# Kernel optimization log

Hardware: AMD Instinct MI355X
Metric: run time of the kernel (lower is better)

## Reference

```python
import jax, jax.numpy as jnp
import numpy as np

NUM_HEADS = 8
AREA = 4
EPS = 1e-5  # torch BatchNorm2d default


def _conv1x1(x, w):
    # x: [B,C,H,W], w: [O,C] -> [B,O,H,W]
    return jnp.einsum('bchw,oc->bohw', x, w)


def _bn(y, g, b, m, v):
    # inference-mode BatchNorm2d, per-channel affine
    s = g / jnp.sqrt(v + EPS)
    return y * s[None, :, None, None] + (b - m * s)[None, :, None, None]


def setup_inputs() -> dict:
    key = jax.random.key(0)
    ks = jax.random.split(key, 16)
    B, C, H, W = 2, 256, 64, 64
    d = {}
    d['x'] = jax.random.normal(ks[0], (B, C, H, W), jnp.float32)
    # qk conv (dim -> 2*dim) + BN
    d['w_qk'] = jax.random.normal(ks[1], (2 * C, C), jnp.float32) * 0.06
    d['g_qk'] = jax.random.uniform(ks[2], (2 * C,), jnp.float32, 0.5, 1.5)
    d['b_qk'] = jax.random.normal(ks[3], (2 * C,), jnp.float32) * 0.1
    d['m_qk'] = jax.random.normal(ks[4], (2 * C,), jnp.float32) * 0.1
    d['v_qk'] = jax.random.uniform(ks[5], (2 * C,), jnp.float32, 0.5, 1.5)
    # v conv (dim -> dim) + BN
    d['w_v'] = jax.random.normal(ks[6], (C, C), jnp.float32) * 0.06
    d['g_v'] = jax.random.uniform(ks[7], (C,), jnp.float32, 0.5, 1.5)
    d['b_v'] = jax.random.normal(ks[8], (C,), jnp.float32) * 0.1
    d['m_v'] = jax.random.normal(ks[9], (C,), jnp.float32) * 0.1
    d['v_v'] = jax.random.uniform(ks[10], (C,), jnp.float32, 0.5, 1.5)
    # proj conv (dim -> dim) + BN
    d['w_p'] = jax.random.normal(ks[11], (C, C), jnp.float32) * 0.06
    d['g_p'] = jax.random.uniform(ks[12], (C,), jnp.float32, 0.5, 1.5)
    d['b_p'] = jax.random.normal(ks[13], (C,), jnp.float32) * 0.1
    d['m_p'] = jax.random.normal(ks[14], (C,), jnp.float32) * 0.1
    d['v_p'] = jax.random.uniform(ks[15], (C,), jnp.float32, 0.5, 1.5)
    return d


def reference(x, w_qk, g_qk, b_qk, m_qk, v_qk,
              w_v, g_v, b_v, m_v, v_v,
              w_p, g_p, b_p, m_p, v_p):
    B, C, H, W = x.shape
    N = H * W
    hd = C // NUM_HEADS

    qk = _bn(_conv1x1(x, w_qk), g_qk, b_qk, m_qk, v_qk)          # [B,2C,H,W]
    qk = qk.reshape(B, 2 * C, N).transpose(0, 2, 1)               # [B,N,2C]
    vv = _bn(_conv1x1(x, w_v), g_v, b_v, m_v, v_v)                # [B,C,H,W]
    vv = vv.reshape(B, C, N).transpose(0, 2, 1)                   # [B,N,C]

    Ba, Na = B * AREA, N // AREA
    qk = qk.reshape(Ba, Na, 2 * C)
    vv = vv.reshape(Ba, Na, C)
    q, k = qk[..., :C], qk[..., C:]

    # [Ba,Na,C] -> [Ba,heads,hd,Na] (matches torch transpose(1,2).view)
    q = q.reshape(Ba, Na, NUM_HEADS, hd).transpose(0, 2, 3, 1)
    k = k.reshape(Ba, Na, NUM_HEADS, hd).transpose(0, 2, 3, 1)
    v = vv.reshape(Ba, Na, NUM_HEADS, hd).transpose(0, 2, 3, 1)

    scale = hd ** -0.5
    attn = jnp.einsum('bhdi,bhdj->bhij', q, k) * scale            # [Ba,h,Na,Na]
    attn = jax.nn.softmax(attn, axis=-1)                          # max-sub exp/sum
    out = jnp.einsum('bhdj,bhij->bihd', v, attn)                  # [Ba,Na,h,hd]

    out = out.reshape(B, N, C).reshape(B, H, W, C).transpose(0, 3, 1, 2)
    return _bn(_conv1x1(out, w_p), g_p, b_p, m_p, v_p)            # [B,C,H,W]
```

## Files before the change

### kernel.cpp

```cpp
#include <hip/hip_runtime.h>
#include <hip/hip_bf16.h>
#include <math.h>

#define CCH   256
#define NPIX  4096
#define NHD   8
#define HD    32
#define NA    1024
#define BN_EPS 1e-5f
#define ATT_SCALE (0.17677669529663687f * 1.4426950408889634f)

typedef __attribute__((ext_vector_type(8))) short bf16x8;
typedef __attribute__((ext_vector_type(4))) short bf16x4;
typedef __attribute__((ext_vector_type(4))) float f32x4;

static __device__ inline short f2bf(float f) {
    union { float f; unsigned u; } v; v.f = f;
    unsigned r = (v.u + 0x7fff + ((v.u >> 16) & 1)) >> 16;
    return (short)r;
}

static __device__ inline unsigned int pk2bf(float a, float b) {
    __hip_bfloat162 h2 = __float22bfloat162_rn(make_float2(a, b));
    union { __hip_bfloat162 h; unsigned int u; } v; v.h = h2;
    return v.u;
}

__global__ __launch_bounds__(256)
void prep_kernel(const float* __restrict__ x, short* __restrict__ Xt,
                 const float* __restrict__ wqk, const float* __restrict__ wv,
                 const float* __restrict__ wp, short* __restrict__ Wb) {
    __shared__ short tile[64][66];
    const int t = threadIdx.x;
    const int z = blockIdx.z;
    if (z == 2) {
        const int id  = blockIdx.y * 64 + blockIdx.x;
        const int idx = (id * 256 + t) * 4;
        const float* src; int off;
        if (idx < 131072)      { src = wqk; off = idx; }
        else if (idx < 196608) { src = wv;  off = idx - 131072; }
        else                   { src = wp;  off = idx - 196608; }
        const float4 v = *(const float4*)(src + off);
        short4 o;
        o.x = f2bf(v.x); o.y = f2bf(v.y); o.z = f2bf(v.z); o.w = f2bf(v.w);
        *(short4*)(Wb + idx) = o;
        return;
    }
    const int n0 = blockIdx.x << 6;
    const int c0 = blockIdx.y << 6;
    const int b  = z;
    const float* xp = x + (((size_t)(b * CCH + c0)) << 12) + n0;
    #pragma unroll
    for (int j = 0; j < 16; ++j) {
        const int lin = (j << 8) + t;
        const int cl = lin >> 6, nl = lin & 63;
        tile[cl][nl] = f2bf(xp[((size_t)cl << 12) + nl]);
    }
    __syncthreads();
    short* xtp = Xt + ((((size_t)b << 12) + n0) << 8) + c0;
    #pragma unroll
    for (int j = 0; j < 16; ++j) {
        const int lin = (j << 8) + t;
        const int nl = lin >> 6, cl = lin & 63;
        xtp[((size_t)nl << 8) + cl] = tile[cl][nl];
    }
}

__global__ __launch_bounds__(256)
void qkv_gemm(const short* __restrict__ Xt, const short* __restrict__ Wb,
              const float* __restrict__ g_qk, const float* __restrict__ b_qk,
              const float* __restrict__ m_qk, const float* __restrict__ v_qk,
              const float* __restrict__ g_v, const float* __restrict__ b_v,
              const float* __restrict__ m_v, const float* __restrict__ v_v,
              short* __restrict__ Qb, short* __restrict__ Kb,
              short* __restrict__ Vb) {
    __shared__ short A_lds[128][72];
    __shared__ short B_lds[64][72];
    const int t    = threadIdx.x;
    const int lane = t & 63;
    const int w    = t >> 6;
    const int c    = lane & 15;
    const int quad = lane >> 4;
    const int wm   = w >> 1;
    const int wn   = w & 1;
    const int m0 = blockIdx.x * 128;
    const int n0 = blockIdx.y * 64 + wn * 32;

    const int rowS = t >> 3;
    const int kc   = t & 7;
    const short* gA0 = Xt + (size_t)(m0 + rowS) * 256 + kc * 8;
    const short* gA1 = gA0 + 32 * 256;
    const short* gA2 = gA0 + 64 * 256;
    const short* gA3 = gA0 + 96 * 256;
    const short* gB0 = Wb + (size_t)(blockIdx.y * 64 + rowS) * 256 + kc * 8;
    const short* gB1 = gB0 + 32 * 256;
    short* lA0 = &A_lds[rowS][kc * 8];
    short* lA1 = &A_lds[rowS + 32][kc * 8];
    short* lA2 = &A_lds[rowS + 64][kc * 8];
    short* lA3 = &A_lds[rowS + 96][kc * 8];
    short* lB0 = &B_lds[rowS][kc * 8];
    short* lB1 = &B_lds[rowS + 32][kc * 8];

    f32x4 acc[4][2];
    #pragma unroll
    for (int f = 0; f < 4; ++f)
        #pragma unroll
        for (int g = 0; g < 2; ++g) acc[f][g] = (f32x4){0.f, 0.f, 0.f, 0.f};

    #pragma unroll
    for (int kt = 0; kt < 4; ++kt) {
        const int k0 = kt * 64;
        bf16x8 a0 = *(const bf16x8*)(gA0 + k0);
        bf16x8 a1 = *(const bf16x8*)(gA1 + k0);
        bf16x8 a2 = *(const bf16x8*)(gA2 + k0);
        bf16x8 a3 = *(const bf16x8*)(gA3 + k0);
        bf16x8 b0 = *(const bf16x8*)(gB0 + k0);
        bf16x8 b1 = *(const bf16x8*)(gB1 + k0);
        if (kt) __syncthreads();
        *(bf16x8*)lA0 = a0;
        *(bf16x8*)lA1 = a1;
        *(bf16x8*)lA2 = a2;
        *(bf16x8*)lA3 = a3;
        *(bf16x8*)lB0 = b0;
        *(bf16x8*)lB1 = b1;
        __syncthreads();
        #pragma unroll
        for (int s = 0; s < 2; ++s) {
            const int ko = s * 32 + quad * 8;
            bf16x8 af[4], bg[2];
            #pragma unroll
            for (int f = 0; f < 4; ++f)
                af[f] = *(const bf16x8*)&A_lds[wm * 64 + f * 16 + c][ko];
            #pragma unroll
            for (int g = 0; g < 2; ++g)
                bg[g] = *(const bf16x8*)&B_lds[wn * 32 + g * 16 + c][ko];
            #pragma unroll
            for (int f = 0; f < 4; ++f)
                #pragma unroll
                for (int g = 0; g < 2; ++g)
                    acc[f][g] = __builtin_amdgcn_mfma_f32_16x16x32_bf16(af[f], bg[g], acc[f][g], 0, 0, 0);
        }
    }

    const int mw = m0 + wm * 64;
    if (n0 < 512) {
        const bool isQ = (n0 < 256);
        short* dst = isQ ? Qb : Kb;
        const float fold = isQ ? ATT_SCALE : 1.0f;
        #pragma unroll
        for (int g = 0; g < 2; ++g) {
            const int o  = n0 + g * 16 + c;
            const int cd = o & 255;
            const int h  = cd >> 5;
            const int d  = cd & 31;
            float s    = g_qk[o] * rsqrtf(v_qk[o] + BN_EPS);
            float beta = (b_qk[o] - m_qk[o] * s) * fold;
            s *= fold;
            #pragma unroll
            for (int f = 0; f < 4; ++f) {
                #pragma unroll
                for (int r = 0; r < 4; ++r) {
                    const int row  = mw + f * 16 + (quad << 2) + r;
                    const int pair = (row >> 10) * NHD + h;
                    const int i    = row & 1023;
                    dst[(((size_t)pair << 10) + i) * HD + d] = f2bf(acc[f][g][r] * s + beta);
                }
            }
        }
    } else {
        #pragma unroll
        for (int g = 0; g < 2; ++g) {
            const int c2 = n0 + g * 16 + c - 512;
            const int d  = c2 & 31;
            const int hp = c2 >> 5;
            const float s    = g_v[c2] * rsqrtf(v_v[c2] + BN_EPS);
            const float beta = b_v[c2] - m_v[c2] * s;
            #pragma unroll
            for (int f = 0; f < 4; ++f) {
                #pragma unroll
                for (int r = 0; r < 4; ++r) {
                    const int row  = mw + f * 16 + (quad << 2) + r;
                    const int pair = (row >> 10) * NHD + hp;
                    const int j    = row & 1023;
                    Vb[((size_t)pair << 15) + (d << 10) + j] = f2bf(acc[f][g][r] * s + beta);
                }
            }
        }
    }
}

__global__ __launch_bounds__(256, 4)
void attn_kernel(const short* __restrict__ Qb,
                 const short* __restrict__ Kb,
                 const short* __restrict__ Vb,
                 short* __restrict__ AOt) {
    const int tid  = threadIdx.x;
    const int wave = tid >> 6;
    const int lane = tid & 63;
    const int c    = lane & 15;
    const int quad = lane >> 4;
    const int pidx  = wave >> 1;
    const int jhalf = wave & 1;

    const int bx  = blockIdx.x;
    const int hi  = bx >> 3;
    const int p   = (bx & 7) + ((hi >> 4) << 3);
    const int blk = hi & 15;
    const int i0a = (blk << 6) + (pidx << 5);
    const int i0b = i0a + 16;
    const int ba  = p >> 3;
    const int h   = p & 7;

    __shared__ __align__(16) short Klds[2][64][40];
    __shared__ __align__(16) short Vlds[2][32][72];
    __shared__ f32x4 mrgA[2][4][64];
    __shared__ float mrgL[2][2][64];

    const short* qbase = Qb + ((size_t)p << 15);
    const short* kbase = Kb + ((size_t)p << 15);
    const short* vbase = Vb + ((size_t)p << 15);

    bf16x8 qfa = *(const bf16x8*)(qbase + ((i0a + c) << 5) + (quad << 3));
    bf16x8 qfb = *(const bf16x8*)(qbase + ((i0b + c) << 5) + (quad << 3));

    const int krow = tid >> 2;
    const int kkc  = tid & 3;
    const int jj_  = krow >> 5;
    const int r32  = krow & 31;
    const int r16  = r32 & 15;
    const int srcr = ((r16 >> 2) << 3) + (r16 & 3) + ((r32 >> 4) << 2) + (jj_ << 5);
    const short* kS = kbase + (srcr << 5) + kkc * 8;
    short* kD0 = &Klds[0][krow][kkc * 8];
    short* kD1 = &Klds[1][krow][kkc * 8];
    const int vrow = tid >> 3;
    const int vkc  = tid & 7;
    const short* vS = vbase + (vrow << 10) + vkc * 8;
    short* vD0 = &Vlds[0][vrow][vkc * 8];
    short* vD1 = &Vlds[1][vrow][vkc * 8];

    f32x4 acc0a = {0.f,0.f,0.f,0.f}, acc1a = {0.f,0.f,0.f,0.f};
    f32x4 acc0b = {0.f,0.f,0.f,0.f}, acc1b = {0.f,0.f,0.f,0.f};
    float la = 0.f, lb = 0.f;
    const f32x4 zero = {0.f,0.f,0.f,0.f};

    for (int it = 0; it < 8; ++it) {
        const int joff = it << 6;
        bf16x8 k0 = *(const bf16x8*)(kS + (joff << 5));
        bf16x8 k1 = *(const bf16x8*)(kS + ((joff + 512) << 5));
        bf16x8 v0 = *(const bf16x8*)(vS + joff);
        bf16x8 v1 = *(const bf16x8*)(vS + joff + 512);
        if (it) __syncthreads();
        *(bf16x8*)kD0 = k0;
        *(bf16x8*)kD1 = k1;
        *(bf16x8*)vD0 = v0;
        *(bf16x8*)vD1 = v1;
        __syncthreads();

        #pragma unroll
        for (int jj = 0; jj < 2; ++jj) {
            bf16x8 kf0 = *(const bf16x8*)&Klds[jhalf][(jj << 5) + c][quad << 3];
            bf16x8 kf1 = *(const bf16x8*)&Klds[jhalf][(jj << 5) + 16 + c][quad << 3];
            bf16x8 vf0 = *(const bf16x8*)&Vlds[jhalf][c][(jj << 5) + (quad << 3)];
            bf16x8 vf1 = *(const bf16x8*)&Vlds[jhalf][c + 16][(jj << 5) + (quad << 3)];

            f32x4 s0a = __builtin_amdgcn_mfma_f32_16x16x32_bf16(kf0, qfa, zero, 0, 0, 0);
            f32x4 s1a = __builtin_amdgcn_mfma_f32_16x16x32_bf16(kf1, qfa, zero, 0, 0, 0);
            f32x4 s0b = __builtin_amdgcn_mfma_f32_16x16x32_bf16(kf0, qfb, zero, 0, 0, 0);
            f32x4 s1b = __builtin_amdgcn_mfma_f32_16x16x32_bf16(kf1, qfb, zero, 0, 0, 0);

            float p0a[4], p1a[4], p0b[4], p1b[4];
            #pragma unroll
            for (int r = 0; r < 4; ++r) {
                p0a[r] = __builtin_amdgcn_exp2f(s0a[r]);
                p1a[r] = __builtin_amdgcn_exp2f(s1a[r]);
                p0b[r] = __builtin_amdgcn_exp2f(s0b[r]);
                p1b[r] = __builtin_amdgcn_exp2f(s1b[r]);
            }
            la += (p0a[0]+p0a[1]) + (p0a[2]+p0a[3]) + (p1a[0]+p1a[1]) + (p1a[2]+p1a[3]);
            lb += (p0b[0]+p0b[1]) + (p0b[2]+p0b[3]) + (p1b[0]+p1b[1]) + (p1b[2]+p1b[3]);

            union { unsigned int u[4]; bf16x8 v; } pfa, pfb;
            pfa.u[0] = pk2bf(p0a[0], p0a[1]);
            pfa.u[1] = pk2bf(p0a[2], p0a[3]);
            pfa.u[2] = pk2bf(p1a[0], p1a[1]);
            pfa.u[3] = pk2bf(p1a[2], p1a[3]);
            pfb.u[0] = pk2bf(p0b[0], p0b[1]);
            pfb.u[1] = pk2bf(p0b[2], p0b[3]);
            pfb.u[2] = pk2bf(p1b[0], p1b[1]);
            pfb.u[3] = pk2bf(p1b[2], p1b[3]);

            acc0a = __builtin_amdgcn_mfma_f32_16x16x32_bf16(pfa.v, vf0, acc0a, 0, 0, 0);
            acc1a = __builtin_amdgcn_mfma_f32_16x16x32_bf16(pfa.v, vf1, acc1a, 0, 0, 0);
            acc0b = __builtin_amdgcn_mfma_f32_16x16x32_bf16(pfb.v, vf0, acc0b, 0, 0, 0);
            acc1b = __builtin_amdgcn_mfma_f32_16x16x32_bf16(pfb.v, vf1, acc1b, 0, 0, 0);
        }
    }

    __syncthreads();
    if (jhalf == 1) {
        mrgA[pidx][0][lane] = acc0a;
        mrgA[pidx][1][lane] = acc1a;
        mrgA[pidx][2][lane] = acc0b;
        mrgA[pidx][3][lane] = acc1b;
        mrgL[pidx][0][lane] = la;
        mrgL[pidx][1][lane] = lb;
    }
    __syncthreads();
    if (jhalf == 1) return;

    acc0a += mrgA[pidx][0][lane];
    acc1a += mrgA[pidx][1][lane];
    acc0b += mrgA[pidx][2][lane];
    acc1b += mrgA[pidx][3][lane];
    la += mrgL[pidx][0][lane];
    lb += mrgL[pidx][1][lane];

    la += __shfl_xor(la, 16); la += __shfl_xor(la, 32);
    lb += __shfl_xor(lb, 16); lb += __shfl_xor(lb, 32);

    #pragma unroll
    for (int r = 0; r < 4; ++r) {
        const int rr = (quad << 2) + r;
        const float rla = 1.f / __shfl(la, rr, 16);
        const float rlb = 1.f / __shfl(lb, rr, 16);
        const size_t basea = ((((size_t)ba << 10) + i0a + rr) << 8) + (h << 5);
        const size_t baseb = ((((size_t)ba << 10) + i0b + rr) << 8) + (h << 5);
        AOt[basea + c]      = f2bf(acc0a[r] * rla);
        AOt[basea + c + 16] = f2bf(acc1a[r] * rla);
        AOt[baseb + c]      = f2bf(acc0b[r] * rlb);
        AOt[baseb + c + 16] = f2bf(acc1b[r] * rlb);
    }
}

__global__ __launch_bounds__(256)
void pconv_gemm(const short* __restrict__ Wp, const short* __restrict__ AOt,
                const float* __restrict__ g_p, const float* __restrict__ b_p,
                const float* __restrict__ m_p, const float* __restrict__ v_p,
                float* __restrict__ out) {
    __shared__ short A_lds[64][72];
    __shared__ short B_lds[128][72];
    const int t    = threadIdx.x;
    const int lane = t & 63;
    const int w    = t >> 6;
    const int c    = lane & 15;
    const int quad = lane >> 4;
    const int wm   = w >> 1;
    const int wn   = w & 1;
    const int m0 = blockIdx.x * 64;
    const int n0 = blockIdx.y * 128 + wn * 64;

    const int rowS = t >> 3;
    const int kc   = t & 7;
    const short* gA0 = Wp + (size_t)(m0 + rowS) * 256 + kc * 8;
    const short* gA1 = gA0 + 32 * 256;
    const short* gB0 = AOt + (size_t)(blockIdx.y * 128 + rowS) * 256 + kc * 8;
    const short* gB1 = gB0 + 32 * 256;
    const short* gB2 = gB0 + 64 * 256;
    const short* gB3 = gB0 + 96 * 256;
    short* lA0 = &A_lds[rowS][kc * 8];
    short* lA1 = &A_lds[rowS + 32][kc * 8];
    short* lB0 = &B_lds[rowS][kc * 8];
    short* lB1 = &B_lds[rowS + 32][kc * 8];
    short* lB2 = &B_lds[rowS + 64][kc * 8];
    short* lB3 = &B_lds[rowS + 96][kc * 8];

    f32x4 acc[2][4];
    #pragma unroll
    for (int f = 0; f < 2; ++f)
        #pragma unroll
        for (int g = 0; g < 4; ++g) acc[f][g] = (f32x4){0.f, 0.f, 0.f, 0.f};

    #pragma unroll
    for (int kt = 0; kt < 4; ++kt) {
        const int k0 = kt * 64;
        bf16x8 a0 = *(const bf16x8*)(gA0 + k0);
        bf16x8 a1 = *(const bf16x8*)(gA1 + k0);
        bf16x8 b0 = *(const bf16x8*)(gB0 + k0);
        bf16x8 b1 = *(const bf16x8*)(gB1 + k0);
        bf16x8 b2 = *(const bf16x8*)(gB2 + k0);
        bf16x8 b3 = *(const bf16x8*)(gB3 + k0);
        if (kt) __syncthreads();
        *(bf16x8*)lA0 = a0;
        *(bf16x8*)lA1 = a1;
        *(bf16x8*)lB0 = b0;
        *(bf16x8*)lB1 = b1;
        *(bf16x8*)lB2 = b2;
        *(bf16x8*)lB3 = b3;
        __syncthreads();
        #pragma unroll
        for (int s = 0; s < 2; ++s) {
            const int ko = s * 32 + quad * 8;
            bf16x8 af[2], bg[4];
            #pragma unroll
            for (int f = 0; f < 2; ++f)
                af[f] = *(const bf16x8*)&A_lds[wm * 32 + f * 16 + c][ko];
            #pragma unroll
            for (int g = 0; g < 4; ++g)
                bg[g] = *(const bf16x8*)&B_lds[wn * 64 + g * 16 + c][ko];
            #pragma unroll
            for (int f = 0; f < 2; ++f)
                #pragma unroll
                for (int g = 0; g < 4; ++g)
                    acc[f][g] = __builtin_amdgcn_mfma_f32_16x16x32_bf16(af[f], bg[g], acc[f][g], 0, 0, 0);
        }
    }

    const int mw = m0 + wm * 32;
    #pragma unroll
    for (int f = 0; f < 2; ++f) {
        #pragma unroll
        for (int r = 0; r < 4; ++r) {
            const int o = mw + f * 16 + (quad << 2) + r;
            const float s    = g_p[o] * rsqrtf(v_p[o] + BN_EPS);
            const float beta = b_p[o] - m_p[o] * s;
            #pragma unroll
            for (int g = 0; g < 4; ++g) {
                const int col = n0 + g * 16 + c;
                const int b = col >> 12, n = col & 4095;
                out[((size_t)(b * CCH + o) << 12) + n] = acc[f][g][r] * s + beta;
            }
        }
    }
}

extern "C" void kernel_launch(void* const* d_in, const int* in_sizes, int n_in,
                              void* d_out, int out_size, void* d_ws, size_t ws_size,
                              hipStream_t stream) {
    const float* x    = (const float*)d_in[0];
    const float* w_qk = (const float*)d_in[1];
    const float* g_qk = (const float*)d_in[2];
    const float* b_qk = (const float*)d_in[3];
    const float* m_qk = (const float*)d_in[4];
    const float* v_qk = (const float*)d_in[5];
    const float* w_v  = (const float*)d_in[6];
    const float* g_v  = (const float*)d_in[7];
    const float* b_v  = (const float*)d_in[8];
    const float* m_v  = (const float*)d_in[9];
    const float* v_v  = (const float*)d_in[10];
    const float* w_p  = (const float*)d_in[11];
    const float* g_p  = (const float*)d_in[12];
    const float* b_p  = (const float*)d_in[13];
    const float* m_p  = (const float*)d_in[14];
    const float* v_p  = (const float*)d_in[15];

    short* Qb  = (short*)d_ws;
    short* Kb  = Qb + 2097152;
    short* Vb  = Kb + 2097152;
    short* Xt  = Vb + 2097152;
    short* Wb  = Xt + 2097152;
    short* AOt = Xt;

    dim3 gprep(64, 4, 3);
    prep_kernel<<<gprep, 256, 0, stream>>>(x, Xt, w_qk, w_v, w_p, Wb);

    dim3 gqkv(64, 12);
    qkv_gemm<<<gqkv, 256, 0, stream>>>(Xt, Wb, g_qk, b_qk, m_qk, v_qk,
                                       g_v, b_v, m_v, v_v, Qb, Kb, Vb);

    attn_kernel<<<1024, 256, 0, stream>>>(Qb, Kb, Vb, AOt);

    dim3 gp(4, 64);
    pconv_gemm<<<gp, 256, 0, stream>>>(Wb + 768 * 256, AOt, g_p, b_p, m_p, v_p, (float*)d_out);
}
```

Baseline: 122.6 us.

## Use direct global-to-LDS async loads with XOR swizzle in 1x1 conv GEMMs

Replaces the register-staged global→LDS tile copies in the QKV and projection GEMMs with global_load_lds 16-byte direct copies. The padded LDS rows become unpadded 64-wide rows with an XOR swizzle on 16-byte chunks to avoid bank conflicts on the MFMA fragment reads. This is meant to cut VGPR use and instruction overhead in the load path. It relies on the builtin's wave-contiguous LDS write pattern matching the swizzled layout, and there is no explicit wait on the async loads before the barrier.

```diff
diff --git a/kernel.cpp b/kernel.cpp
--- a/kernel.cpp
+++ b/kernel.cpp
@@ -24,6 +24,12 @@
     __hip_bfloat162 h2 = __float22bfloat162_rn(make_float2(a, b));
     union { __hip_bfloat162 h; unsigned int u; } v; v.h = h2;
     return v.u;
+}
+
+static __device__ __forceinline__ void async_copy16(short* lds, const short* g) {
+    __builtin_amdgcn_global_load_lds(
+        (const __attribute__((address_space(1))) unsigned int*)g,
+        (__attribute__((address_space(3))) unsigned int*)lds, 16, 0, 0);
 }
 
 __global__ __launch_bounds__(256)
@@ -74,8 +80,8 @@
               const float* __restrict__ m_v, const float* __restrict__ v_v,
               short* __restrict__ Qb, short* __restrict__ Kb,
               short* __restrict__ Vb) {
-    __shared__ short A_lds[128][72];
-    __shared__ short B_lds[64][72];
+    __shared__ short A_lds[128][64];
+    __shared__ short B_lds[64][64];
     const int t    = threadIdx.x;
     const int lane = t & 63;
     const int w    = t >> 6;
@@ -86,54 +92,44 @@
     const int m0 = blockIdx.x * 128;
     const int n0 = blockIdx.y * 64 + wn * 32;
 
-    const int rowS = t >> 3;
-    const int kc   = t & 7;
-    const short* gA0 = Xt + (size_t)(m0 + rowS) * 256 + kc * 8;
-    const short* gA1 = gA0 + 32 * 256;
-    const short* gA2 = gA0 + 64 * 256;
-    const short* gA3 = gA0 + 96 * 256;
-    const short* gB0 = Wb + (size_t)(blockIdx.y * 64 + rowS) * 256 + kc * 8;
-    const short* gB1 = gB0 + 32 * 256;
-    short* lA0 = &A_lds[rowS][kc * 8];
-    short* lA1 = &A_lds[rowS + 32][kc * 8];
-    short* lA2 = &A_lds[rowS + 64][kc * 8];
-    short* lA3 = &A_lds[rowS + 96][kc * 8];
-    short* lB0 = &B_lds[rowS][kc * 8];
-    short* lB1 = &B_lds[rowS + 32][kc * 8];
+    const int sub = lane >> 3;
+    const int pos = lane & 7;
+    const int sc  = (pos ^ sub) << 3;
+    const short* gA = Xt + (size_t)(m0 + w * 32 + sub) * 256 + sc;
+    const short* gB = Wb + (size_t)(blockIdx.y * 64 + w * 16 + sub) * 256 + sc;
+    short* lA = &A_lds[w * 32][0];
+    short* lB = &B_lds[w * 16][0];
 
     f32x4 acc[4][2];
     #pragma unroll
     for (int f = 0; f < 4; ++f)
         #pragma unroll
         for (int g = 0; g < 2; ++g) acc[f][g] = (f32x4){0.f, 0.f, 0.f, 0.f};
+
+    const int swz = (c & 7);
 
     #pragma unroll
     for (int kt = 0; kt < 4; ++kt) {
         const int k0 = kt * 64;
-        bf16x8 a0 = *(const bf16x8*)(gA0 + k0);
-        bf16x8 a1 = *(const bf16x8*)(gA1 + k0);
-        bf16x8 a2 = *(const bf16x8*)(gA2 + k0);
-        bf16x8 a3 = *(const bf16x8*)(gA3 + k0);
-        bf16x8 b0 = *(const bf16x8*)(gB0 + k0);
-        bf16x8 b1 = *(const bf16x8*)(gB1 + k0);
         if (kt) __syncthreads();
-        *(bf16x8*)lA0 = a0;
-        *(bf16x8*)lA1 = a1;
-        *(bf16x8*)lA2 = a2;
-        *(bf16x8*)lA3 = a3;
-        *(bf16x8*)lB0 = b0;
-        *(bf16x8*)lB1 = b1;
+        #pragma unroll
+        for (int b8 = 0; b8 < 4; ++b8)
+            async_copy16(lA + b8 * 512, gA + b8 * 8 * 256 + k0);
+        #pragma unroll
+        for (int b8 = 0; b8 < 2; ++b8)
+            async_copy16(lB + b8 * 512, gB + b8 * 8 * 256 + k0);
         __syncthreads();
         #pragma unroll
         for (int s = 0; s < 2; ++s) {
-            const int ko = s * 32 + quad * 8;
+            const int q   = s * 4 + quad;
+            const int col = (q ^ swz) << 3;
             bf16x8 af[4], bg[2];
             #pragma unroll
             for (int f = 0; f < 4; ++f)
-                af[f] = *(const bf16x8*)&A_lds[wm * 64 + f * 16 + c][ko];
+                af[f] = *(const bf16x8*)&A_lds[wm * 64 + f * 16 + c][col];
             #pragma unroll
             for (int g = 0; g < 2; ++g)
-                bg[g] = *(const bf16x8*)&B_lds[wn * 32 + g * 16 + c][ko];
+                bg[g] = *(const bf16x8*)&B_lds[wn * 32 + g * 16 + c][col];
             #pragma unroll
             for (int f = 0; f < 4; ++f)
                 #pragma unroll
@@ -337,8 +333,8 @@
                 const float* __restrict__ g_p, const float* __restrict__ b_p,
                 const float* __restrict__ m_p, const float* __restrict__ v_p,
                 float* __restrict__ out) {
-    __shared__ short A_lds[64][72];
-    __shared__ short B_lds[128][72];
+    __shared__ short A_lds[64][64];
+    __shared__ short B_lds[128][64];
     const int t    = threadIdx.x;
     const int lane = t & 63;
     const int w    = t >> 6;
@@ -349,54 +345,44 @@
     const int m0 = blockIdx.x * 64;
     const int n0 = blockIdx.y * 128 + wn * 64;
 
-    const int rowS = t >> 3;
-    const int kc   = t & 7;
-    const short* gA0 = Wp + (size_t)(m0 + rowS) * 256 + kc * 8;
-    const short* gA1 = gA0 + 32 * 256;
-    const short* gB0 = AOt + (size_t)(blockIdx.y * 128 + rowS) * 256 + kc * 8;
-    const short* gB1 = gB0 + 32 * 256;
-    const short* gB2 = gB0 + 64 * 256;
-    const short* gB3 = gB0 + 96 * 256;
-    short* lA0 = &A_lds[rowS][kc * 8];
-    short* lA1 = &A_lds[rowS + 32][kc * 8];
-    short* lB0 = &B_lds[rowS][kc * 8];
-    short* lB1 = &B_lds[rowS + 32][kc * 8];
-    short* lB2 = &B_lds[rowS + 64][kc * 8];
-    short* lB3 = &B_lds[rowS + 96][kc * 8];
+    const int sub = lane >> 3;
+    const int pos = lane & 7;
+    const int sc  = (pos ^ sub) << 3;
+    const short* gA = Wp + (size_t)(m0 + w * 16 + sub) * 256 + sc;
+    const short* gB = AOt + (size_t)(blockIdx.y * 128 + w * 32 + sub) * 256 + sc;
+    short* lA = &A_lds[w * 16][0];
+    short* lB = &B_lds[w * 32][0];
 
     f32x4 acc[2][4];
     #pragma unroll
     for (int f = 0; f < 2; ++f)
         #pragma unroll
         for (int g = 0; g < 4; ++g) acc[f][g] = (f32x4){0.f, 0.f, 0.f, 0.f};
+
+    const int swz = (c & 7);
 
     #pragma unroll
     for (int kt = 0; kt < 4; ++kt) {
         const int k0 = kt * 64;
-        bf16x8 a0 = *(const bf16x8*)(gA0 + k0);
-        bf16x8 a1 = *(const bf16x8*)(gA1 + k0);
-        bf16x8 b0 = *(const bf16x8*)(gB0 + k0);
-        bf16x8 b1 = *(const bf16x8*)(gB1 + k0);
-        bf16x8 b2 = *(const bf16x8*)(gB2 + k0);
-        bf16x8 b3 = *(const bf16x8*)(gB3 + k0);
         if (kt) __syncthreads();
-        *(bf16x8*)lA0 = a0;
-        *(bf16x8*)lA1 = a1;
-        *(bf16x8*)lB0 = b0;
-        *(bf16x8*)lB1 = b1;
-        *(bf16x8*)lB2 = b2;
-        *(bf16x8*)lB3 = b3;
+        #pragma unroll
+        for (int b8 = 0; b8 < 2; ++b8)
+            async_copy16(lA + b8 * 512, gA + b8 * 8 * 256 + k0);
+        #pragma unroll
+        for (int b8 = 0; b8 < 4; ++b8)
+            async_copy16(lB + b8 * 512, gB + b8 * 8 * 256 + k0);
         __syncthreads();
         #pragma unroll
         for (int s = 0; s < 2; ++s) {
-            const int ko = s * 32 + quad * 8;
+            const int q   = s * 4 + quad;
+            const int col = (q ^ swz) << 3;
             bf16x8 af[2], bg[4];
             #pragma unroll
             for (int f = 0; f < 2; ++f)
-                af[f] = *(const bf16x8*)&A_lds[wm * 32 + f * 16 + c][ko];
+                af[f] = *(const bf16x8*)&A_lds[wm * 32 + f * 16 + c][col];
             #pragma unroll
             for (int g = 0; g < 4; ++g)
-                bg[g] = *(const bf16x8*)&B_lds[wn * 64 + g * 16 + c][ko];
+                bg[g] = *(const bf16x8*)&B_lds[wn * 64 + g * 16 + c][col];
             #pragma unroll
             for (int f = 0; f < 2; ++f)
                 #pragma unroll
```

After: 123.0 us. About the same (+0.3%).
